# Performance work log

Hardware: AMD Instinct MI355X
Metric: run time of the kernel (lower is better)

The kernel has to match this reference:

```python
import jax, jax.numpy as jnp
import numpy as np

HIDDEN = 1024
HEADS = 16
B, L = 2, 2048


def _xavier(key, shape):
    fan_in, fan_out = shape[1], shape[0]
    limit = float(np.sqrt(6.0 / (fan_in + fan_out)))
    return jax.random.uniform(key, shape, jnp.float32, -limit, limit)


def setup_inputs() -> dict:
    key = jax.random.key(0)
    ks = jax.random.split(key, 6)
    return {
        "query": jax.random.normal(ks[0], (B, L, HIDDEN), jnp.float32),
        "bias": jax.random.normal(ks[1], (B, 1, 1, L), jnp.float32),
        "Wq": _xavier(ks[2], (HIDDEN, HIDDEN)), "bq": jnp.zeros((HIDDEN,), jnp.float32),
        "Wk": _xavier(ks[3], (HIDDEN, HIDDEN)), "bk": jnp.zeros((HIDDEN,), jnp.float32),
        "Wv": _xavier(ks[4], (HIDDEN, HIDDEN)), "bv": jnp.zeros((HIDDEN,), jnp.float32),
        "Wo": _xavier(ks[5], (HIDDEN, HIDDEN)), "bo": jnp.zeros((HIDDEN,), jnp.float32),
    }


def _split_heads(x):
    b, l, c = x.shape
    return x.reshape(b, l, HEADS, c // HEADS).transpose(0, 2, 1, 3)  # [B,H,L,d]


def reference(query, bias, Wq, bq, Wk, bk, Wv, bv, Wo, bo):
    d_head = HIDDEN // HEADS
    q = query @ Wq.T + bq
    k = query @ Wk.T + bk
    v = query @ Wv.T + bv
    q = _split_heads(q) * (d_head ** -0.5)  # [B,H,L,d]
    k = _split_heads(k)
    v = _split_heads(v)
    logits = jnp.einsum("bhqd,bhkd->bhqk", q, k) + bias  # [B,H,L,L]
    weights = jax.nn.softmax(logits, axis=-1)
    x = jnp.einsum("bhqk,bhkd->bhqd", weights, v)  # [B,H,L,d]
    x = x.transpose(0, 2, 1, 3).reshape(query.shape[0], query.shape[1], HIDDEN)
    return x @ Wo.T + bo
```

## Files before the change

### kernel.cpp

```cpp
#include <hip/hip_runtime.h>
#include <hip/hip_fp16.h>
#include <stdint.h>

#define HIDDEN 1024
#define HEADS  16
#define DH     64
#define B_     2
#define L_     2048
#define M_TOT  (B_ * L_)
#define ELEMS  (M_TOT * HIDDEN)
#define LOG2E  1.44269504088896340736f

typedef _Float16 f16;
typedef _Float16 f16x4 __attribute__((ext_vector_type(4)));
typedef _Float16 f16x8 __attribute__((ext_vector_type(8)));
typedef float    f32x4 __attribute__((ext_vector_type(4)));
typedef uint32_t u32;
typedef __attribute__((address_space(1))) u32 gu32;
typedef __attribute__((address_space(3))) u32 su32;

#define MFMA32(a, b, c) __builtin_amdgcn_mfma_f32_16x16x32_f16(a, b, c, 0, 0, 0)


__global__ __launch_bounds__(256)
void convert_f16(const float* __restrict__ query,
                 const float* __restrict__ Wq, const float* __restrict__ Wk,
                 const float* __restrict__ Wv, const float* __restrict__ Wo,
                 f16* __restrict__ Qh, f16* __restrict__ Wh)
{
    const int NQ4 = ELEMS / 4;
    const int NW4 = (HIDDEN * HIDDEN) / 4;
    const int total = NQ4 + 4 * NW4;
    for (int u = blockIdx.x * 256 + threadIdx.x; u < total; u += gridDim.x * 256) {
        float4 v; f16* dp;
        if (u < NQ4) {
            v = ((const float4*)query)[u];
            dp = Qh + (size_t)u * 4;
        } else {
            const int u2 = u - NQ4;
            const int w = u2 >> 18;
            const int off = u2 & (NW4 - 1);
            const float* W = (w == 0) ? Wq : (w == 1) ? Wk : (w == 2) ? Wv : Wo;
            v = ((const float4*)W)[off];
            dp = Wh + (size_t)u2 * 4;
        }
        f16x4 h = { (f16)v.x, (f16)v.y, (f16)v.z, (f16)v.w };
        *(f16x4*)dp = h;
    }
}

template<int TM, int TN>
__device__ __forceinline__
void gemm_loop(const f16* __restrict__ A, const f16* __restrict__ W,
               int mb, int nb, f32x4 (&acc)[TM / 32][TN / 32])
{
    __shared__ f16 As[2][TM * 32];
    __shared__ f16 Bs[2][TN * 32];

    const int tid  = threadIdx.x;
    const int lane = tid & 63;
    const int wave = tid >> 6;
    const int quad = lane >> 4;
    const int l16  = lane & 15;
    const int wm   = (wave >> 1) * (TM / 2);
    const int wn   = (wave & 1) * (TN / 2);

    constexpr int AISS = TM / 64;
    constexpr int BISS = TN / 64;
    int aoff[AISS], boff[BISS];
#pragma unroll
    for (int q = 0; q < AISS; q++) {
        const int p16 = (wave * AISS + q) * 64 + lane;
        const int r = p16 >> 2;
        const int c8 = (p16 & 3) ^ ((r >> 1) & 3);
        aoff[q] = (mb + r) * HIDDEN + c8 * 8;
    }
#pragma unroll
    for (int q = 0; q < BISS; q++) {
        const int p16 = (wave * BISS + q) * 64 + lane;
        const int r = p16 >> 2;
        const int c8 = (p16 & 3) ^ ((r >> 1) & 3);
        boff[q] = (nb + r) * HIDDEN + c8 * 8;
    }

#pragma unroll
    for (int q = 0; q < AISS; q++)
        __builtin_amdgcn_global_load_lds((gu32*)&A[aoff[q]],
                                         (su32*)&As[0][(wave * AISS + q) * 512], 16, 0, 0);
#pragma unroll
    for (int q = 0; q < BISS; q++)
        __builtin_amdgcn_global_load_lds((gu32*)&W[boff[q]],
                                         (su32*)&Bs[0][(wave * BISS + q) * 512], 16, 0, 0);
    __syncthreads();

    for (int kb = 0; kb < HIDDEN; kb += 32) {
        const int buf = (kb >> 5) & 1;
        const int nkb = (kb + 32 < HIDDEN) ? kb + 32 : 0;

#pragma unroll
        for (int q = 0; q < AISS; q++)
            __builtin_amdgcn_global_load_lds((gu32*)&A[aoff[q] + nkb],
                                             (su32*)&As[buf ^ 1][(wave * AISS + q) * 512], 16, 0, 0);
#pragma unroll
        for (int q = 0; q < BISS; q++)
            __builtin_amdgcn_global_load_lds((gu32*)&W[boff[q] + nkb],
                                             (su32*)&Bs[buf ^ 1][(wave * BISS + q) * 512], 16, 0, 0);

        f16x8 af[TM / 32], bf[TN / 32];
#pragma unroll
        for (int i = 0; i < TM / 32; i++) {
            const int r = wm + i * 16 + l16;
            af[i] = *(const f16x8*)&As[buf][r * 32 + (quad ^ ((r >> 1) & 3)) * 8];
        }
#pragma unroll
        for (int j = 0; j < TN / 32; j++) {
            const int r = wn + j * 16 + l16;
            bf[j] = *(const f16x8*)&Bs[buf][r * 32 + (quad ^ ((r >> 1) & 3)) * 8];
        }
#pragma unroll
        for (int i = 0; i < TM / 32; i++)
#pragma unroll
            for (int j = 0; j < TN / 32; j++)
                acc[i][j] = MFMA32(af[i], bf[j], acc[i][j]);
        __syncthreads();
    }
}

__global__ __launch_bounds__(256)
void proj_qkv(const f16* __restrict__ A, const f16* __restrict__ W,
              const float* __restrict__ bq, const float* __restrict__ bk,
              const float* __restrict__ bv,
              f16* __restrict__ Qo, f16* __restrict__ Ko, f16* __restrict__ Vo)
{
    f32x4 acc[4][4] = {};
    const int mb = blockIdx.x * 128, nb = blockIdx.y * 128;
    gemm_loop<128, 128>(A, W, mb, nb, acc);

    const int lane = threadIdx.x & 63, wave = threadIdx.x >> 6;
    const int quad = lane >> 4, l16 = lane & 15;
    const int wm = (wave >> 1) * 64, wn = (wave & 1) * 64;
    const int nsel = nb >> 10;
    const int nbase = nb & 1023;

    if (nsel < 2) {
        const float* bias = nsel ? bk : bq;
        f16* out = nsel ? Ko : Qo;
        const float scale = nsel ? 1.0f : 0.125f * LOG2E;
#pragma unroll
        for (int i = 0; i < 4; i++)
#pragma unroll
            for (int j = 0; j < 4; j++) {
                const int n1 = nbase + wn + j * 16 + l16;
                const float bn = bias[n1];
                const int h = n1 >> 6, dd = n1 & 63;
#pragma unroll
                for (int r = 0; r < 4; r++) {
                    const int m = mb + wm + i * 16 + quad * 4 + r;
                    const int b = m >> 11, l = m & (L_ - 1);
                    out[(((b * HEADS + h) * L_) + l) * DH + dd] =
                        (f16)((acc[i][j][r] + bn) * scale);
                }
            }
    } else {
#pragma unroll
        for (int i = 0; i < 4; i++)
#pragma unroll
            for (int j = 0; j < 4; j++) {
                const int n1 = nbase + wn + j * 16 + l16;
                const float bn = bv[n1];
                const int h = n1 >> 6, dd = n1 & 63;
                const int m0 = mb + wm + i * 16 + quad * 4;
                const int b = m0 >> 11, l0 = m0 & (L_ - 1);
                f16x4 pk;
#pragma unroll
                for (int r = 0; r < 4; r++) pk[r] = (f16)(acc[i][j][r] + bn);
                *(f16x4*)&Vo[((size_t)(b * HEADS + h) * DH + dd) * L_ + l0] = pk;
            }
    }
}

__global__ __launch_bounds__(256)
void proj_out(const f16* __restrict__ A, const f16* __restrict__ W,
              const float* __restrict__ bo, float* __restrict__ out)
{
    f32x4 acc[4][2] = {};
    const int mb = blockIdx.x * 128, nb = blockIdx.y * 64;
    gemm_loop<128, 64>(A, W, mb, nb, acc);

    const int lane = threadIdx.x & 63, wave = threadIdx.x >> 6;
    const int quad = lane >> 4, l16 = lane & 15;
    const int wm = (wave >> 1) * 64, wn = (wave & 1) * 32;
#pragma unroll
    for (int i = 0; i < 4; i++)
#pragma unroll
        for (int j = 0; j < 2; j++) {
            const int n = nb + wn + j * 16 + l16;
            const float bn = bo[n];
#pragma unroll
            for (int r = 0; r < 4; r++) {
                const int m = mb + wm + i * 16 + quad * 4 + r;
                out[m * HIDDEN + n] = acc[i][j][r] + bn;
            }
        }
}

__global__ __launch_bounds__(256)
void attn(const f16* __restrict__ Q, const f16* __restrict__ K,
          const f16* __restrict__ Vt, const float* __restrict__ bias,
          f16* __restrict__ X)
{
    __shared__ f16 Ks[2][64 * 64];
    __shared__ f16 Vs[2][64 * 64];
    __shared__ float biasl[L_];

    const int tid  = threadIdx.x;
    const int lane = tid & 63;
    const int wave = tid >> 6;
    const int quad = lane >> 4;
    const int l16  = lane & 15;

    const int bid = (int)blockIdx.x;
    const int lb  = (bid & 7) * 64 + (bid >> 3);
    const int bh = lb >> 4;
    const int b  = bh >> 4, h = bh & 15;
    const int qrow0 = (lb & 15) * 128 + wave * 32;

    const f16* Qh  = Q  + (size_t)bh * L_ * DH;
    const f16* Kh  = K  + (size_t)bh * L_ * DH;
    const f16* Vth = Vt + (size_t)bh * DH * L_;

    {
        const float4* bb = (const float4*)(bias + b * L_);
        for (int i = tid; i < L_ / 4; i += 256) {
            const float4 v = bb[i];
            biasl[i * 4 + 0] = v.x * LOG2E;
            biasl[i * 4 + 1] = v.y * LOG2E;
            biasl[i * 4 + 2] = v.z * LOG2E;
            biasl[i * 4 + 3] = v.w * LOG2E;
        }
    }

    int krow[2], kcol[2], vcol[2];
#pragma unroll
    for (int q = 0; q < 2; q++) {
        const int p = (wave * 2 + q) * 64 + lane;
        const int r = p >> 3;
        const int w = p & 7;
        krow[q] = r;
        kcol[q] = (w ^ (r & 7) ^ (((r >> 3) & 1) << 2)) * 8;
        vcol[q] = (w ^ (r & 7)) * 8;
    }

    f16x8 qf[2][2];
#pragma unroll
    for (int qt = 0; qt < 2; qt++)
#pragma unroll
        for (int hh = 0; hh < 2; hh++)
            qf[qt][hh] = *(const f16x8*)&Qh[(qrow0 + qt * 16 + l16) * DH + hh * 32 + quad * 8];

    int koffX[2][2], koffY[2][2], voff[2][4];
#pragma unroll
    for (int g = 0; g < 2; g++) {
        const int rX = g * 32 + ((l16 >> 2) << 3) + (l16 & 3);
        const int rY = rX + 4;
        const int gkX = (rX & 7) ^ (((rX >> 3) & 1) << 2);
        const int gkY = (rY & 7) ^ (((rY >> 3) & 1) << 2);
#pragma unroll
        for (int hh = 0; hh < 2; hh++) {
            koffX[g][hh] = rX * 64 + (((hh * 4 + quad) ^ gkX) << 3);
            koffY[g][hh] = rY * 64 + (((hh * 4 + quad) ^ gkY) << 3);
        }
#pragma unroll
        for (int t = 0; t < 4; t++) {
            const int vr = t * 16 + l16;
            voff[g][t] = vr * 64 + (((g * 4 + quad) ^ (vr & 7)) << 3);
        }
    }

#pragma unroll
    for (int q = 0; q < 2; q++) {
        __builtin_amdgcn_global_load_lds((gu32*)(Kh + (size_t)krow[q] * DH + kcol[q]),
                                         (su32*)&Ks[0][(wave * 2 + q) * 512], 16, 0, 0);
        __builtin_amdgcn_global_load_lds((gu32*)(Vth + (size_t)krow[q] * L_ + vcol[q]),
                                         (su32*)&Vs[0][(wave * 2 + q) * 512], 16, 0, 0);
    }

    f32x4 o[2][4] = {};
    f32x4 osum[2] = {};
    const f16x8 ones8 = { (f16)1.f, (f16)1.f, (f16)1.f, (f16)1.f,
                          (f16)1.f, (f16)1.f, (f16)1.f, (f16)1.f };
    __syncthreads();

#pragma unroll 1
    for (int kb = 0; kb < L_; kb += 64) {
        const int buf = (kb >> 6) & 1;
        const int nkb = (kb + 64 < L_) ? kb + 64 : 0;

#pragma unroll
        for (int q = 0; q < 2; q++) {
            __builtin_amdgcn_global_load_lds(
                (gu32*)(Kh + (size_t)(nkb + krow[q]) * DH + kcol[q]),
                (su32*)&Ks[buf ^ 1][(wave * 2 + q) * 512], 16, 0, 0);
            __builtin_amdgcn_global_load_lds(
                (gu32*)(Vth + (size_t)krow[q] * L_ + nkb + vcol[q]),
                (su32*)&Vs[buf ^ 1][(wave * 2 + q) * 512], 16, 0, 0);
        }

#pragma unroll
        for (int g = 0; g < 2; g++) {
            const f16x8 kx0 = *(const f16x8*)&Ks[buf][koffX[g][0]];
            const f16x8 kx1 = *(const f16x8*)&Ks[buf][koffX[g][1]];
            const f16x8 ky0 = *(const f16x8*)&Ks[buf][koffY[g][0]];
            const f16x8 ky1 = *(const f16x8*)&Ks[buf][koffY[g][1]];
            f16x8 va[4];
#pragma unroll
            for (int t = 0; t < 4; t++)
                va[t] = *(const f16x8*)&Vs[buf][voff[g][t]];
            const f32x4 blvX = *(const f32x4*)&biasl[kb + g * 32 + quad * 8];
            const f32x4 blvY = *(const f32x4*)&biasl[kb + g * 32 + quad * 8 + 4];

#pragma unroll
            for (int qt = 0; qt < 2; qt++) {
                f32x4 zx = blvX, zy = blvY;
                zx = MFMA32(kx0, qf[qt][0], zx);
                zx = MFMA32(kx1, qf[qt][1], zx);
                zy = MFMA32(ky0, qf[qt][0], zy);
                zy = MFMA32(ky1, qf[qt][1], zy);
                const f16x8 pb = {
                    (f16)__builtin_amdgcn_exp2f(zx[0]), (f16)__builtin_amdgcn_exp2f(zx[1]),
                    (f16)__builtin_amdgcn_exp2f(zx[2]), (f16)__builtin_amdgcn_exp2f(zx[3]),
                    (f16)__builtin_amdgcn_exp2f(zy[0]), (f16)__builtin_amdgcn_exp2f(zy[1]),
                    (f16)__builtin_amdgcn_exp2f(zy[2]), (f16)__builtin_amdgcn_exp2f(zy[3]) };
#pragma unroll
                for (int t = 0; t < 4; t++)
                    o[qt][t] = MFMA32(va[t], pb, o[qt][t]);
                osum[qt] = MFMA32(ones8, pb, osum[qt]);
            }
        }
        __syncthreads();
    }

#pragma unroll
    for (int qt = 0; qt < 2; qt++) {
        const float inv = 1.0f / osum[qt][0];
        const size_t qrow = (size_t)b * L_ + qrow0 + qt * 16 + l16;
#pragma unroll
        for (int t = 0; t < 4; t++) {
            f16x4 pk;
#pragma unroll
            for (int r = 0; r < 4; r++) pk[r] = (f16)(o[qt][t][r] * inv);
            *(f16x4*)&X[qrow * HIDDEN + h * DH + t * 16 + quad * 4] = pk;
        }
    }
}

extern "C" void kernel_launch(void* const* d_in, const int* in_sizes, int n_in,
                              void* d_out, int out_size, void* d_ws, size_t ws_size,
                              hipStream_t stream)
{
    const float* query = (const float*)d_in[0];
    const float* bias  = (const float*)d_in[1];
    const float* Wq = (const float*)d_in[2]; const float* bq = (const float*)d_in[3];
    const float* Wk = (const float*)d_in[4]; const float* bk = (const float*)d_in[5];
    const float* Wv = (const float*)d_in[6]; const float* bv = (const float*)d_in[7];
    const float* Wo = (const float*)d_in[8]; const float* bo = (const float*)d_in[9];
    float* out = (float*)d_out;

    f16* Wh = (f16*)d_ws;
    f16* Qh = Wh + 4096 * 1024;
    f16* Kf = Qh + ELEMS;
    f16* Vf = Kf + ELEMS;
    f16* Qf = Vf + ELEMS;
    f16* Xf = Qh;

    convert_f16<<<2048, 256, 0, stream>>>(query, Wq, Wk, Wv, Wo, Qh, Wh);
    proj_qkv<<<dim3(32, 24), 256, 0, stream>>>(Qh, Wh, bq, bk, bv, Qf, Kf, Vf);
    attn<<<512, 256, 0, stream>>>(Qf, Kf, Vf, bias, Xf);
    proj_out<<<dim3(32, 16), 256, 0, stream>>>(Xf, Wh + 3072 * 1024, bo, out);
}
```

Before: 202.7 us.

## Deepen attention K/V prefetch to a 4-stage LDS ring with manual waitcnt

Replaces the double-buffered K/V LDS staging in the attention kernel with a four-buffer ring that keeps three tiles in flight. A partial vmcnt wait plus a single raw barrier per iteration replaces the two __syncthreads, and s_setprio raises wave priority during the MFMA section. The aim is to hide more global-load latency and cut synchronisation cost. In exchange the kernel uses twice the LDS for K/V, which may lower occupancy, and correctness now depends on the hand-written vmcnt counts matching the number of outstanding loads.

```diff
diff --git a/kernel.cpp b/kernel.cpp
--- a/kernel.cpp
+++ b/kernel.cpp
@@ -209,8 +209,8 @@
           const f16* __restrict__ Vt, const float* __restrict__ bias,
           f16* __restrict__ X)
 {
-    __shared__ f16 Ks[2][64 * 64];
-    __shared__ f16 Vs[2][64 * 64];
+    __shared__ f16 Ks[4][64 * 64];
+    __shared__ f16 Vs[4][64 * 64];
     __shared__ float biasl[L_];
 
     const int tid  = threadIdx.x;
@@ -221,8 +221,8 @@
 
     const int bid = (int)blockIdx.x;
     const int lb  = (bid & 7) * 64 + (bid >> 3);
-    const int bh = lb >> 4;
-    const int b  = bh >> 4, h = bh & 15;
+    const int bh  = lb >> 4;
+    const int b   = bh >> 4, h = bh & 15;
     const int qrow0 = (lb & 15) * 128 + wave * 32;
 
     const f16* Qh  = Q  + (size_t)bh * L_ * DH;
@@ -257,6 +257,7 @@
 #pragma unroll
         for (int hh = 0; hh < 2; hh++)
             qf[qt][hh] = *(const f16x8*)&Qh[(qrow0 + qt * 16 + l16) * DH + hh * 32 + quad * 8];
+    asm volatile("" :: "v"(qf[0][0]), "v"(qf[0][1]), "v"(qf[1][0]), "v"(qf[1][1]));
 
     int koffX[2][2], koffY[2][2], voff[2][4];
 #pragma unroll
@@ -277,45 +278,57 @@
         }
     }
 
-#pragma unroll
-    for (int q = 0; q < 2; q++) {
-        __builtin_amdgcn_global_load_lds((gu32*)(Kh + (size_t)krow[q] * DH + kcol[q]),
-                                         (su32*)&Ks[0][(wave * 2 + q) * 512], 16, 0, 0);
-        __builtin_amdgcn_global_load_lds((gu32*)(Vth + (size_t)krow[q] * L_ + vcol[q]),
-                                         (su32*)&Vs[0][(wave * 2 + q) * 512], 16, 0, 0);
-    }
+    asm volatile("s_waitcnt lgkmcnt(0)" ::: "memory");
+
+#pragma unroll
+    for (int p = 0; p < 3; p++)
+#pragma unroll
+        for (int q = 0; q < 2; q++) {
+            __builtin_amdgcn_global_load_lds(
+                (gu32*)(Kh + (size_t)(p * 64 + krow[q]) * DH + kcol[q]),
+                (su32*)&Ks[p][(wave * 2 + q) * 512], 16, 0, 0);
+            __builtin_amdgcn_global_load_lds(
+                (gu32*)(Vth + (size_t)krow[q] * L_ + p * 64 + vcol[q]),
+                (su32*)&Vs[p][(wave * 2 + q) * 512], 16, 0, 0);
+        }
 
     f32x4 o[2][4] = {};
     f32x4 osum[2] = {};
     const f16x8 ones8 = { (f16)1.f, (f16)1.f, (f16)1.f, (f16)1.f,
                           (f16)1.f, (f16)1.f, (f16)1.f, (f16)1.f };
-    __syncthreads();
 
 #pragma unroll 1
     for (int kb = 0; kb < L_; kb += 64) {
-        const int buf = (kb >> 6) & 1;
-        const int nkb = (kb + 64 < L_) ? kb + 64 : 0;
-
+        const int t = kb >> 6;
+        asm volatile("s_waitcnt vmcnt(8)" ::: "memory");
+        __builtin_amdgcn_s_barrier();
+        __builtin_amdgcn_sched_barrier(0);
+
+        const int nt = (t + 3 < 32) ? t + 3 : 0;
 #pragma unroll
         for (int q = 0; q < 2; q++) {
             __builtin_amdgcn_global_load_lds(
-                (gu32*)(Kh + (size_t)(nkb + krow[q]) * DH + kcol[q]),
-                (su32*)&Ks[buf ^ 1][(wave * 2 + q) * 512], 16, 0, 0);
+                (gu32*)(Kh + (size_t)(nt * 64 + krow[q]) * DH + kcol[q]),
+                (su32*)&Ks[(t + 3) & 3][(wave * 2 + q) * 512], 16, 0, 0);
             __builtin_amdgcn_global_load_lds(
-                (gu32*)(Vth + (size_t)krow[q] * L_ + nkb + vcol[q]),
-                (su32*)&Vs[buf ^ 1][(wave * 2 + q) * 512], 16, 0, 0);
-        }
-
+                (gu32*)(Vth + (size_t)krow[q] * L_ + nt * 64 + vcol[q]),
+                (su32*)&Vs[(t + 3) & 3][(wave * 2 + q) * 512], 16, 0, 0);
+        }
+
+        const f16* Kb = &Ks[t & 3][0];
+        const f16* Vb = &Vs[t & 3][0];
+
+        __builtin_amdgcn_s_setprio(1);
 #pragma unroll
         for (int g = 0; g < 2; g++) {
-            const f16x8 kx0 = *(const f16x8*)&Ks[buf][koffX[g][0]];
-            const f16x8 kx1 = *(const f16x8*)&Ks[buf][koffX[g][1]];
-            const f16x8 ky0 = *(const f16x8*)&Ks[buf][koffY[g][0]];
-            const f16x8 ky1 = *(const f16x8*)&Ks[buf][koffY[g][1]];
+            const f16x8 kx0 = *(const f16x8*)&Kb[koffX[g][0]];
+            const f16x8 kx1 = *(const f16x8*)&Kb[koffX[g][1]];
+            const f16x8 ky0 = *(const f16x8*)&Kb[koffY[g][0]];
+            const f16x8 ky1 = *(const f16x8*)&Kb[koffY[g][1]];
             f16x8 va[4];
 #pragma unroll
-            for (int t = 0; t < 4; t++)
-                va[t] = *(const f16x8*)&Vs[buf][voff[g][t]];
+            for (int v4 = 0; v4 < 4; v4++)
+                va[v4] = *(const f16x8*)&Vb[voff[g][v4]];
             const f32x4 blvX = *(const f32x4*)&biasl[kb + g * 32 + quad * 8];
             const f32x4 blvY = *(const f32x4*)&biasl[kb + g * 32 + quad * 8 + 4];
 
@@ -332,13 +345,15 @@
                     (f16)__builtin_amdgcn_exp2f(zy[0]), (f16)__builtin_amdgcn_exp2f(zy[1]),
                     (f16)__builtin_amdgcn_exp2f(zy[2]), (f16)__builtin_amdgcn_exp2f(zy[3]) };
 #pragma unroll
-                for (int t = 0; t < 4; t++)
-                    o[qt][t] = MFMA32(va[t], pb, o[qt][t]);
+                for (int v4 = 0; v4 < 4; v4++)
+                    o[qt][v4] = MFMA32(va[v4], pb, o[qt][v4]);
                 osum[qt] = MFMA32(ones8, pb, osum[qt]);
             }
         }
-        __syncthreads();
-    }
+        __builtin_amdgcn_s_setprio(0);
+    }
+
+    asm volatile("s_waitcnt vmcnt(0)" ::: "memory");
 
 #pragma unroll
     for (int qt = 0; qt < 2; qt++) {
```

Measured after the change: 196.6 us. 1.03x faster.
